# Optimization experiments

Hardware: AMD Instinct MI355X
Metric: run time of the kernel (lower is better)

## Reference

```python
import jax, jax.numpy as jnp
import numpy as np

B, S, D, H, FF = 2, 2048, 512, 8, 2048
DK = D // H
EPS = 1e-5


def layer_norm(x, g, b):
    mu = jnp.mean(x, axis=-1, keepdims=True)
    var = jnp.mean((x - mu) ** 2, axis=-1, keepdims=True)
    return (x - mu) / jnp.sqrt(var + EPS) * g + b


def split_heads(x):  # [B,S,D] -> [B,H,S,DK]
    b, s, _ = x.shape
    return x.reshape(b, s, H, DK).transpose(0, 2, 1, 3)


def merge_heads(x):  # [B,H,S,DK] -> [B,S,D]
    b, h, s, dk = x.shape
    return x.transpose(0, 2, 1, 3).reshape(b, s, h * dk)


def mha(q_in, kv, in_w, in_b, out_w, out_b):
    # torch nn.MultiheadAttention, batch_first, eval mode (no dropout)
    Wq, Wk, Wv = in_w[:D], in_w[D:2 * D], in_w[2 * D:]
    bq, bk, bv = in_b[:D], in_b[D:2 * D], in_b[2 * D:]
    q = split_heads(q_in @ Wq.T + bq)
    k = split_heads(kv @ Wk.T + bk)
    v = split_heads(kv @ Wv.T + bv)
    scores = jnp.einsum('bhqd,bhkd->bhqk', q, k) / jnp.sqrt(jnp.float32(DK))
    attn = jax.nn.softmax(scores, axis=-1)
    out = merge_heads(jnp.einsum('bhqk,bhkd->bhqd', attn, v))
    return out @ out_w.T + out_b


def setup_inputs() -> dict:
    key = jax.random.key(0)
    ks = jax.random.split(key, 32)
    p = lambda k, shape: (jax.random.normal(k, shape, jnp.float32) * 0.02)
    inp = {
        'x_q': jax.random.normal(ks[0], (B, S, D), jnp.float32),
        'x1': jax.random.normal(ks[1], (B, S, D), jnp.float32),
        'x2': jax.random.normal(ks[2], (B, S, D), jnp.float32),
        # causal self-attention projections (no output proj in original)
        'sa_wq': p(ks[3], (D, D)), 'sa_bq': jnp.zeros((D,), jnp.float32),
        'sa_wk': p(ks[4], (D, D)), 'sa_bk': jnp.zeros((D,), jnp.float32),
        'sa_wv': p(ks[5], (D, D)), 'sa_bv': jnp.zeros((D,), jnp.float32),
        'ln1_g': jnp.ones((D,), jnp.float32), 'ln1_b': jnp.zeros((D,), jnp.float32),
        # shared cross-attention (cross_attn used twice in forward)
        'mha_in_w': p(ks[6], (3 * D, D)), 'mha_in_b': jnp.zeros((3 * D,), jnp.float32),
        'mha_out_w': p(ks[7], (D, D)), 'mha_out_b': jnp.zeros((D,), jnp.float32),
        # shared add_norm2 (used twice)
        'ln2_g': jnp.ones((D,), jnp.float32), 'ln2_b': jnp.zeros((D,), jnp.float32),
        # FFN
        'ffn_w1': p(ks[8], (FF, D)), 'ffn_b1': jnp.zeros((FF,), jnp.float32),
        'ffn_w2': p(ks[9], (D, FF)), 'ffn_b2': jnp.zeros((D,), jnp.float32),
        # add_norm3 (final)
        'ln3_g': jnp.ones((D,), jnp.float32), 'ln3_b': jnp.zeros((D,), jnp.float32),
    }
    return inp


def reference(x_q, x1, x2, sa_wq, sa_bq, sa_wk, sa_bk, sa_wv, sa_bv,
              ln1_g, ln1_b, mha_in_w, mha_in_b, mha_out_w, mha_out_b,
              ln2_g, ln2_b, ffn_w1, ffn_b1, ffn_w2, ffn_b2, ln3_g, ln3_b):
    # --- causal self-attention (hand-rolled, masked_fill with -1e9) ---
    q = split_heads(x_q @ sa_wq.T + sa_bq)
    k = split_heads(x_q @ sa_wk.T + sa_bk)
    v = split_heads(x_q @ sa_wv.T + sa_bv)
    scores = jnp.einsum('bhqd,bhkd->bhqk', q, k) / jnp.sqrt(jnp.float32(DK))
    causal = jnp.tril(jnp.ones((S, S), dtype=bool))
    scores = jnp.where(causal[None, None], scores, jnp.float32(-1e9))
    attn = jax.nn.softmax(scores, axis=-1)
    y_sa = merge_heads(jnp.einsum('bhqk,bhkd->bhqd', attn, v))
    y = layer_norm(x_q + y_sa, ln1_g, ln1_b)
    # --- cross-attention 1 (shared weights) + shared add_norm2 ---
    yattn = mha(y, x1, mha_in_w, mha_in_b, mha_out_w, mha_out_b)
    yattn = layer_norm(y + yattn, ln2_g, ln2_b)
    # --- cross-attention 2 (SAME module/weights as cross-attn 1) ---
    yattn2 = mha(yattn, x2, mha_in_w, mha_in_b, mha_out_w, mha_out_b)
    yattn2 = layer_norm(yattn + yattn2, ln2_g, ln2_b)
    # --- FFN + add_norm3 ---
    h = jax.nn.relu(yattn2 @ ffn_w1.T + ffn_b1)
    ff = h @ ffn_w2.T + ffn_b2
    return layer_norm(yattn2 + ff, ln3_g, ln3_b)
```

## Files before the change

### kernel.cpp

```cpp
#include <hip/hip_runtime.h>
#include <hip/hip_bf16.h>

#define S_LEN 2048
#define DMODEL 512
#define NHEAD 8
#define DKH 64
#define FFDIM 2048
#define BATCH 2
#define NROWS (BATCH * S_LEN)

using bf16 = __hip_bfloat16;
typedef __bf16 bf16x8 __attribute__((ext_vector_type(8)));
typedef float floatx4 __attribute__((ext_vector_type(4)));
typedef float floatx16 __attribute__((ext_vector_type(16)));

__device__ inline unsigned short f2bf_bits(float f) {
    union { float f; unsigned u; } c; c.f = f;
    return (unsigned short)((c.u + 0x7FFFu + ((c.u >> 16) & 1u)) >> 16);
}
__device__ inline unsigned pack2bf(float a, float b) {
    return (unsigned)f2bf_bits(a) | ((unsigned)f2bf_bits(b) << 16);
}
__device__ inline unsigned pk2(float a, float b) {
    float2 f; f.x = a; f.y = b;
    __hip_bfloat162 h = __float22bfloat162_rn(f);
    return *(unsigned*)&h;
}

__device__ __forceinline__ void gload_lds16(const bf16* g, bf16* l) {
    __builtin_amdgcn_global_load_lds(
        (const __attribute__((address_space(1))) void*)(const void*)g,
        (__attribute__((address_space(3))) void*)(void*)l, 16, 0, 0);
}

struct CvtSeg { const float* s; bf16* d; int n4; };
struct CvtDesc { CvtSeg seg[12]; };

__launch_bounds__(256)
__global__ void cvt_f32_bf16(CvtDesc desc) {
    const CvtSeg sg = desc.seg[blockIdx.y];
    const int stride = gridDim.x * 256;
    for (int i = blockIdx.x * 256 + threadIdx.x; i < sg.n4; i += stride) {
        const float4 v = ((const float4*)sg.s)[i];
        uint2 o;
        o.x = pack2bf(v.x, v.y);
        o.y = pack2bf(v.z, v.w);
        ((uint2*)sg.d)[i] = o;
    }
}

struct Epi {
    bf16*  outB[3];
    float* outF[3];
    const float* bias[3];
    float scale[3];
    const bf16* A2;
    int a2slab;
    int shift;
    int relu;
};

template <int BM, int BN>
__launch_bounds__(256)
__global__ void gemm2(const bf16* __restrict__ A, const bf16* __restrict__ W,
                      Epi epi, int K)
{
    constexpr int WR = BM / 32;
    constexpr int WC = BN / 32;
    constexpr int SA = BM / 16;
    constexpr int SB = BN / 16;
    constexpr int NG = 2 * (SA + SB);

    __shared__ alignas(16) bf16 As[2][BM][32];
    __shared__ alignas(16) bf16 Bs[2][BN][32];

    const int t = threadIdx.x;
    const int w = t >> 6;
    const int lane = t & 63;
    const int r16 = lane & 15;
    const int quad = lane >> 4;
    const int wm = w >> 1, wn = w & 1;
    const int m0 = blockIdx.x * BM;
    const int n0 = blockIdx.y * BN;

    const bf16* Ause = (epi.A2 && ((n0 >> epi.shift) >= epi.a2slab)) ? epi.A2 : A;

    floatx4 acc[WR][WC];
#pragma unroll
    for (int i = 0; i < WR; i++)
#pragma unroll
        for (int j = 0; j < WC; j++)
#pragma unroll
            for (int e = 0; e < 4; e++) acc[i][j][e] = 0.0f;

    const int grow = lane >> 2;
    const int gcol = (lane & 3) * 8;

    for (int k0 = 0; k0 < K; k0 += 64) {
        __syncthreads();
#pragma unroll
        for (int s = 0; s < NG; s += 4) {
            int sg = s + w;
            int p = 0;
            if (sg >= SA + SB) { p = 1; sg -= SA + SB; }
            const bf16* src;
            bf16* dst;
            if (sg < SA) {
                src = Ause + (size_t)(m0 + sg * 16 + grow) * K + k0 + 32 * p + gcol;
                dst = &As[p][sg * 16][0] + lane * 8;
            } else {
                const int sb = sg - SA;
                src = W + (size_t)(n0 + sb * 16 + grow) * K + k0 + 32 * p + gcol;
                dst = &Bs[p][sb * 16][0] + lane * 8;
            }
            gload_lds16(src, dst);
        }
        __syncthreads();

        bf16x8 af[2][WR], bfr[2][WC];
#pragma unroll
        for (int p = 0; p < 2; p++) {
#pragma unroll
            for (int i = 0; i < WR; i++)
                af[p][i] = *(const bf16x8*)&As[p][wm * (BM / 2) + 16 * i + r16][quad * 8];
#pragma unroll
            for (int j = 0; j < WC; j++)
                bfr[p][j] = *(const bf16x8*)&Bs[p][wn * (BN / 2) + 16 * j + r16][quad * 8];
        }
#pragma unroll
        for (int p = 0; p < 2; p++)
#pragma unroll
            for (int i = 0; i < WR; i++)
#pragma unroll
                for (int j = 0; j < WC; j++)
                    acc[i][j] = __builtin_amdgcn_mfma_f32_16x16x32_bf16(af[p][i], bfr[p][j], acc[i][j], 0, 0, 0);
    }

    const int mask = (1 << epi.shift) - 1;
#pragma unroll
    for (int j = 0; j < WC; j++) {
        const int colb = n0 + wn * (BN / 2) + 16 * j;
        const int sel = __builtin_amdgcn_readfirstlane(colb >> epi.shift);
        const int lcol = (colb & mask) + r16;
        const int ldw = mask + 1;
        const float bv = epi.bias[sel] ? epi.bias[sel][lcol] : 0.0f;
        const float sc = epi.scale[sel];
        bf16* ob = epi.outB[sel];
        float* of = epi.outF[sel];
#pragma unroll
        for (int i = 0; i < WR; i++) {
            const int rowb = m0 + wm * (BM / 2) + 16 * i + 4 * quad;
#pragma unroll
            for (int e = 0; e < 4; e++) {
                float v = (acc[i][j][e] + bv) * sc;
                if (epi.relu) v = fmaxf(v, 0.0f);
                const size_t idx = (size_t)(rowb + e) * ldw + lcol;
                if (of) of[idx] = v;
                if (ob) ob[idx] = __float2bfloat16(v);
            }
        }
    }
}

#define PST 72

__launch_bounds__(256)
__global__ void attn_mfma(const bf16* __restrict__ Qh, const bf16* __restrict__ Kh,
                          const bf16* __restrict__ Vh,
                          float* __restrict__ outF, bf16* __restrict__ outB,
                          int causal)
{
    __shared__ alignas(16) char smem[36864];
    typedef bf16 (*VtT)[64][PST];
    typedef bf16 (*PsT)[32][PST];
    VtT Vt = (VtT)smem;
    PsT Ps = (PsT)(smem + 18432);
    typedef float (*MshT)[64][34];
    MshT Msh = (MshT)smem;

    const int t = threadIdx.x;
    const int w = t >> 6;
    const int lane = t & 63;
    const int c32 = lane & 31;
    const int hi = lane >> 5;
    const int pair = t >> 7;
    const int qg = w & 1;
    const int pl = t & 127;
    const int bh = blockIdx.y;
    const int b = bh >> 3, h = bh & 7;
    const int q0 = blockIdx.x * 64;
    const size_t rowbase = (size_t)b * S_LEN;
    const int hoff = h * DKH;

    bf16x8 qf[4];
    {
        const bf16* qp = Qh + (rowbase + q0 + 32 * qg + c32) * DMODEL + hoff + 8 * hi;
#pragma unroll
        for (int tt = 0; tt < 4; tt++) qf[tt] = *(const bf16x8*)(qp + 16 * tt);
    }

    floatx16 o0, o1;
#pragma unroll
    for (int e = 0; e < 16; e++) { o0[e] = 0.0f; o1[e] = 0.0f; }
    float m = -3e38f, l = 0.0f;

    const int rq = pl & 15;
    const int c8 = ((pl >> 4) & 7) * 8;

    const int nchunk = causal ? (q0 / 64 + 1) : (S_LEN / 64);
    const int nIter = (nchunk + 1) >> 1;

    bf16x8 kf0[4], kf1[4];
    if (pair < nchunk) {
        const bf16* kp = Kh + (rowbase + pair * 64 + c32) * DMODEL + hoff + 8 * hi;
#pragma unroll
        for (int tt = 0; tt < 4; tt++) {
            kf0[tt] = *(const bf16x8*)(kp + 16 * tt);
            kf1[tt] = *(const bf16x8*)(kp + (size_t)32 * DMODEL + 16 * tt);
        }
    }

    for (int it = 0; it < nIter; it++) {
        const int ch = 2 * it + pair;
        const bool active = ch < nchunk;
        const int kb = ch * 64;
        __syncthreads();
        if (active) {
            union { uint4 u; unsigned short s[8]; } r0, r1, r2, r3;
            const bf16* vb = Vh + (rowbase + kb + 4 * rq) * DMODEL + hoff + c8;
            r0.u = *(const uint4*)(vb);
            r1.u = *(const uint4*)(vb + DMODEL);
            r2.u = *(const uint4*)(vb + 2 * DMODEL);
            r3.u = *(const uint4*)(vb + 3 * DMODEL);
#pragma unroll
            for (int j = 0; j < 8; j++) {
                ushort4 pk = { r0.s[j], r1.s[j], r2.s[j], r3.s[j] };
                *(ushort4*)&Vt[pair][c8 + j][4 * rq] = pk;
            }
        }

        if (active) {
            floatx16 s0, s1;
#pragma unroll
            for (int e = 0; e < 16; e++) { s0[e] = 0.0f; s1[e] = 0.0f; }
#pragma unroll
            for (int tt = 0; tt < 4; tt++) {
                s0 = __builtin_amdgcn_mfma_f32_32x32x16_bf16(kf0[tt], qf[tt], s0, 0, 0, 0);
                s1 = __builtin_amdgcn_mfma_f32_32x32x16_bf16(kf1[tt], qf[tt], s1, 0, 0, 0);
            }

            const int chn = ch + 2;
            if (chn < nchunk) {
                const bf16* kp = Kh + (rowbase + chn * 64 + c32) * DMODEL + hoff + 8 * hi;
#pragma unroll
                for (int tt = 0; tt < 4; tt++) {
                    kf0[tt] = *(const bf16x8*)(kp + 16 * tt);
                    kf1[tt] = *(const bf16x8*)(kp + (size_t)32 * DMODEL + 16 * tt);
                }
            }

            if (causal && kb == q0) {
                const int qq = 32 * qg + c32;
#pragma unroll
                for (int r = 0; r < 16; r++) {
                    const int kl = (r & 3) + 8 * (r >> 2) + 4 * hi;
                    if (kl > qq) s0[r] = -3e38f;
                    if (kl + 32 > qq) s1[r] = -3e38f;
                }
            }

            float mc = -3e38f;
#pragma unroll
            for (int r = 0; r < 16; r++) mc = fmaxf(mc, fmaxf(s0[r], s1[r]));
            mc = fmaxf(mc, __shfl_xor(mc, 32, 64));
            const float mold = m;
            const float mn = fmaxf(m, mc);
            const float alpha = __expf(mold - mn);
            m = mn;

            float lc = 0.0f;
#pragma unroll
            for (int g = 0; g < 4; g++) {
                float p0 = __expf(s0[4 * g + 0] - mn), p1 = __expf(s0[4 * g + 1] - mn);
                float p2 = __expf(s0[4 * g + 2] - mn), p3 = __expf(s0[4 * g + 3] - mn);
                lc += (p0 + p1) + (p2 + p3);
                uint2 pw; pw.x = pk2(p0, p1); pw.y = pk2(p2, p3);
                *(uint2*)&Ps[w][c32][8 * g + 4 * hi] = pw;
                p0 = __expf(s1[4 * g + 0] - mn); p1 = __expf(s1[4 * g + 1] - mn);
                p2 = __expf(s1[4 * g + 2] - mn); p3 = __expf(s1[4 * g + 3] - mn);
                lc += (p0 + p1) + (p2 + p3);
                uint2 pw1; pw1.x = pk2(p0, p1); pw1.y = pk2(p2, p3);
                *(uint2*)&Ps[w][c32][32 + 8 * g + 4 * hi] = pw1;
            }
            lc += __shfl_xor(lc, 32, 64);
            l = l * alpha + lc;

            if (!__all(mn == mold)) {
#pragma unroll
                for (int r = 0; r < 16; r++) {
                    const float a = __shfl(alpha, (r & 3) + 8 * (r >> 2) + 4 * hi, 64);
                    o0[r] *= a; o1[r] *= a;
                }
            }
        }

        __syncthreads();

        if (active) {
#pragma unroll
            for (int tt = 0; tt < 4; tt++) {
                const bf16x8 pf = *(const bf16x8*)&Ps[w][c32][16 * tt + 8 * hi];
                const bf16x8 v0 = *(const bf16x8*)&Vt[pair][c32][16 * tt + 8 * hi];
                const bf16x8 v1 = *(const bf16x8*)&Vt[pair][32 + c32][16 * tt + 8 * hi];
                o0 = __builtin_amdgcn_mfma_f32_32x32x16_bf16(pf, v0, o0, 0, 0, 0);
                o1 = __builtin_amdgcn_mfma_f32_32x32x16_bf16(pf, v1, o1, 0, 0, 0);
            }
        }
    }

    __syncthreads();
    if (pair == 1) {
        float* dst = &Msh[qg][lane][0];
        dst[0] = m; dst[1] = l;
#pragma unroll
        for (int r = 0; r < 16; r++) { dst[2 + r] = o0[r]; dst[18 + r] = o1[r]; }
    }
    __syncthreads();
    if (pair == 0) {
        const float* src = &Msh[qg][lane][0];
        const float m_b = src[0], l_b = src[1];
        const float mt = fmaxf(m, m_b);
        const float sA = __expf(m - mt);
        const float sB = __expf(m_b - mt);
        const float lt = l * sA + l_b * sB;
#pragma unroll
        for (int r = 0; r < 16; r++) {
            const int ql = (r & 3) + 8 * (r >> 2) + 4 * hi;
            const float sAr = __shfl(sA, ql, 64);
            const float sBr = __shfl(sB, ql, 64);
            const float li = 1.0f / __shfl(lt, ql, 64);
            const float v0 = (o0[r] * sAr + src[2 + r] * sBr) * li;
            const float v1 = (o1[r] * sAr + src[18 + r] * sBr) * li;
            const size_t idx = (rowbase + q0 + 32 * qg + ql) * DMODEL + hoff + c32;
            if (outF) { outF[idx] = v0; outF[idx + 32] = v1; }
            if (outB) { outB[idx] = __float2bfloat16(v0); outB[idx + 32] = __float2bfloat16(v1); }
        }
    }
}

__launch_bounds__(256)
__global__ void ln_kernel(const float* __restrict__ xmain,
                          const float* __restrict__ resF, const bf16* __restrict__ resB,
                          const float* __restrict__ g, const float* __restrict__ bb,
                          float* __restrict__ outF, bf16* __restrict__ outB)
{
    const int row = blockIdx.x;
    const int t = threadIdx.x;
    const size_t base = (size_t)row * DMODEL;

    float x0 = xmain[base + t];
    float x1 = xmain[base + t + 256];
    if (resF) { x0 += resF[base + t]; x1 += resF[base + t + 256]; }
    if (resB) { x0 += __bfloat162float(resB[base + t]); x1 += __bfloat162float(resB[base + t + 256]); }

    __shared__ float sred[4];
    float s = x0 + x1;
#pragma unroll
    for (int off = 32; off > 0; off >>= 1) s += __shfl_down(s, off);
    if ((t & 63) == 0) sred[t >> 6] = s;
    __syncthreads();
    const float mu = (sred[0] + sred[1] + sred[2] + sred[3]) * (1.0f / DMODEL);

    const float d0 = x0 - mu, d1 = x1 - mu;
    float sv = d0 * d0 + d1 * d1;
#pragma unroll
    for (int off = 32; off > 0; off >>= 1) sv += __shfl_down(sv, off);
    __syncthreads();
    if ((t & 63) == 0) sred[t >> 6] = sv;
    __syncthreads();
    const float var = (sred[0] + sred[1] + sred[2] + sred[3]) * (1.0f / DMODEL);
    const float rstd = rsqrtf(var + 1e-5f);

    const float y0 = d0 * rstd * g[t] + bb[t];
    const float y1 = d1 * rstd * g[t + 256] + bb[t + 256];
    if (outF) { outF[base + t] = y0; outF[base + t + 256] = y1; }
    if (outB) { outB[base + t] = __float2bfloat16(y0); outB[base + t + 256] = __float2bfloat16(y1); }
}

extern "C" void kernel_launch(void* const* d_in, const int* in_sizes, int n_in,
                              void* d_out, int out_size, void* d_ws, size_t ws_size,
                              hipStream_t stream)
{
    const float* x_q       = (const float*)d_in[0];
    const float* x1        = (const float*)d_in[1];
    const float* x2        = (const float*)d_in[2];
    const float* sa_wq     = (const float*)d_in[3];
    const float* sa_bq     = (const float*)d_in[4];
    const float* sa_wk     = (const float*)d_in[5];
    const float* sa_bk     = (const float*)d_in[6];
    const float* sa_wv     = (const float*)d_in[7];
    const float* sa_bv     = (const float*)d_in[8];
    const float* ln1_g     = (const float*)d_in[9];
    const float* ln1_b     = (const float*)d_in[10];
    const float* mha_in_w  = (const float*)d_in[11];
    const float* mha_in_b  = (const float*)d_in[12];
    const float* mha_out_w = (const float*)d_in[13];
    const float* mha_out_b = (const float*)d_in[14];
    const float* ln2_g     = (const float*)d_in[15];
    const float* ln2_b     = (const float*)d_in[16];
    const float* ffn_w1    = (const float*)d_in[17];
    const float* ffn_b1    = (const float*)d_in[18];
    const float* ffn_w2    = (const float*)d_in[19];
    const float* ffn_b2    = (const float*)d_in[20];
    const float* ln3_g     = (const float*)d_in[21];
    const float* ln3_b     = (const float*)d_in[22];

    char* ws = (char*)d_ws;
    const size_t MB = 1024 * 1024;
    const size_t KB = 1024;
    bf16*  q16  = (bf16*)(ws + 0 * MB);
    bf16*  k16  = (bf16*)(ws + 4 * MB);
    bf16*  v16  = (bf16*)(ws + 8 * MB);
    bf16*  a16  = (bf16*)(ws + 12 * MB);
    float* tmp  = (float*)(ws + 16 * MB);
    bf16*  y16  = (bf16*)(ws + 24 * MB);
    bf16*  ya16 = (bf16*)(ws + 28 * MB);
    bf16*  ya2  = (bf16*)(ws + 32 * MB);
    bf16*  xq16 = (bf16*)(ws + 36 * MB);
    bf16*  x116 = (bf16*)(ws + 40 * MB);
    bf16*  x216 = (bf16*)(ws + 44 * MB);
    bf16*  w_sa_qkv = (bf16*)(ws + 48 * MB);
    bf16*  w_in   = (bf16*)(ws + 49 * MB + 512 * KB);
    bf16*  w_out  = (bf16*)(ws + 51 * MB);
    bf16*  w_f1   = (bf16*)(ws + 51 * MB + 512 * KB);
    bf16*  w_f2   = (bf16*)(ws + 53 * MB + 512 * KB);
    bf16*  h16    = (bf16*)(ws + 0 * MB);

    const int DD = DMODEL * DMODEL;
    CvtDesc cd;
    cd.seg[0]  = { x_q,       xq16,        (NROWS * DMODEL) / 4 };
    cd.seg[1]  = { x1,        x116,        (NROWS * DMODEL) / 4 };
    cd.seg[2]  = { x2,        x216,        (NROWS * DMODEL) / 4 };
    cd.seg[3]  = { sa_wq,     w_sa_qkv,           DD / 4 };
    cd.seg[4]  = { sa_wk,     w_sa_qkv + DD,      DD / 4 };
    cd.seg[5]  = { sa_wv,     w_sa_qkv + 2 * DD,  DD / 4 };
    cd.seg[6]  = { mha_in_w,  w_in,   3 * DD / 4 };
    cd.seg[7]  = { mha_out_w, w_out,  DD / 4 };
    cd.seg[8]  = { ffn_w1,    w_f1,   (FFDIM * DMODEL) / 4 };
    cd.seg[9]  = { ffn_w2,    w_f2,   (FFDIM * DMODEL) / 4 };
    cd.seg[10] = { x_q,       xq16,   0 };
    cd.seg[11] = { x_q,       xq16,   0 };
    cvt_f32_bf16<<<dim3(64, 10), 256, 0, stream>>>(cd);

    const dim3 blk(256);
    const dim3 agrid(S_LEN / 64, BATCH * NHEAD);

    Epi eQKV = {};
    eQKV.outB[0] = q16; eQKV.outB[1] = k16; eQKV.outB[2] = v16;
    eQKV.bias[0] = sa_bq; eQKV.bias[1] = sa_bk; eQKV.bias[2] = sa_bv;
    eQKV.scale[0] = 0.125f; eQKV.scale[1] = 1.0f; eQKV.scale[2] = 1.0f;
    eQKV.shift = 9;

    Epi eX1 = {};
    eX1.outB[0] = q16; eX1.outB[1] = k16; eX1.outB[2] = v16;
    eX1.bias[0] = mha_in_b; eX1.bias[1] = mha_in_b + DMODEL; eX1.bias[2] = mha_in_b + 2 * DMODEL;
    eX1.scale[0] = 0.125f; eX1.scale[1] = 1.0f; eX1.scale[2] = 1.0f;
    eX1.A2 = x116; eX1.a2slab = 1; eX1.shift = 9;

    Epi eX2 = eX1;
    eX2.A2 = x216;

    Epi eOut = {};
    eOut.outF[0] = tmp; eOut.bias[0] = mha_out_b; eOut.scale[0] = 1.0f; eOut.shift = 9;

    Epi eF1 = {};
    eF1.outB[0] = h16; eF1.bias[0] = ffn_b1; eF1.scale[0] = 1.0f;
    eF1.shift = 11; eF1.relu = 1;

    Epi eF2 = {};
    eF2.outF[0] = tmp; eF2.bias[0] = ffn_b2; eF2.scale[0] = 1.0f; eF2.shift = 9;

    gemm2<64, 64><<<dim3(64, 24), blk, 0, stream>>>(xq16, w_sa_qkv, eQKV, DMODEL);
    attn_mfma<<<agrid, blk, 0, stream>>>(q16, k16, v16, tmp, nullptr, 1);
    ln_kernel<<<NROWS, blk, 0, stream>>>(tmp, x_q, nullptr, ln1_g, ln1_b, nullptr, y16);

    gemm2<64, 64><<<dim3(64, 24), blk, 0, stream>>>(y16, w_in, eX1, DMODEL);
    attn_mfma<<<agrid, blk, 0, stream>>>(q16, k16, v16, nullptr, a16, 0);
    gemm2<64, 64><<<dim3(64, 8), blk, 0, stream>>>(a16, w_out, eOut, DMODEL);
    ln_kernel<<<NROWS, blk, 0, stream>>>(tmp, nullptr, y16, ln2_g, ln2_b, nullptr, ya16);

    gemm2<64, 64><<<dim3(64, 24), blk, 0, stream>>>(ya16, w_in, eX2, DMODEL);
    attn_mfma<<<agrid, blk, 0, stream>>>(q16, k16, v16, nullptr, a16, 0);
    gemm2<64, 64><<<dim3(64, 8), blk, 0, stream>>>(a16, w_out, eOut, DMODEL);
    ln_kernel<<<NROWS, blk, 0, stream>>>(tmp, nullptr, ya16, ln2_g, ln2_b, nullptr, ya2);

    gemm2<128, 128><<<dim3(32, 16), blk, 0, stream>>>(ya2, w_f1, eF1, DMODEL);
    gemm2<64, 64><<<dim3(64, 8), blk, 0, stream>>>(h16, w_f2, eF2, FFDIM);
    ln_kernel<<<NROWS, blk, 0, stream>>>(tmp, nullptr, ya2, ln3_g, ln3_b, (float*)d_out, nullptr);
}
```

Measured before the change: 447.5 us.

## Split attention key chunks across four wave pairs and keep softmax probabilities in registers

The attention kernel now runs 512 threads, so four wave pairs each process every fourth 64-key chunk, and their partial softmax states are merged in two rounds through shared memory. The P tile no longer goes through LDS: probabilities are packed to bf16 and rearranged across lanes with v_permlane32_swap to form the MFMA operand directly. The softmax switches to exp2 with log2(e) folded into the Q scale, and rescaling is skipped unless the running max grows by more than 8. MFMA sections are wrapped in s_setprio. This adds more merge work and more register pressure, and relies on the lane permutation matching the MFMA operand layout.

```diff
diff --git a/kernel.cpp b/kernel.cpp
--- a/kernel.cpp
+++ b/kernel.cpp
@@ -25,6 +25,9 @@
     float2 f; f.x = a; f.y = b;
     __hip_bfloat162 h = __float22bfloat162_rn(f);
     return *(unsigned*)&h;
+}
+__device__ inline void pl32swap(unsigned &a, unsigned &b) {
+    asm volatile("v_permlane32_swap_b32 %0, %1" : "+v"(a), "+v"(b));
 }
 
 __device__ __forceinline__ void gload_lds16(const bf16* g, bf16* l) {
@@ -164,7 +167,7 @@
 
 #define PST 72
 
-__launch_bounds__(256)
+__launch_bounds__(512, 4)
 __global__ void attn_mfma(const bf16* __restrict__ Qh, const bf16* __restrict__ Kh,
                           const bf16* __restrict__ Vh,
                           float* __restrict__ outF, bf16* __restrict__ outB,
@@ -172,10 +175,8 @@
 {
     __shared__ alignas(16) char smem[36864];
     typedef bf16 (*VtT)[64][PST];
-    typedef bf16 (*PsT)[32][PST];
     VtT Vt = (VtT)smem;
-    PsT Ps = (PsT)(smem + 18432);
-    typedef float (*MshT)[64][34];
+    typedef float (*MshT)[2][64][34];
     MshT Msh = (MshT)smem;
 
     const int t = threadIdx.x;
@@ -208,7 +209,7 @@
     const int c8 = ((pl >> 4) & 7) * 8;
 
     const int nchunk = causal ? (q0 / 64 + 1) : (S_LEN / 64);
-    const int nIter = (nchunk + 1) >> 1;
+    const int nIter = (nchunk + 3) >> 2;
 
     bf16x8 kf0[4], kf1[4];
     if (pair < nchunk) {
@@ -221,7 +222,7 @@
     }
 
     for (int it = 0; it < nIter; it++) {
-        const int ch = 2 * it + pair;
+        const int ch = 4 * it + pair;
         const bool active = ch < nchunk;
         const int kb = ch * 64;
         __syncthreads();
@@ -239,17 +240,20 @@
             }
         }
 
+        unsigned pw[16];
         if (active) {
             floatx16 s0, s1;
 #pragma unroll
             for (int e = 0; e < 16; e++) { s0[e] = 0.0f; s1[e] = 0.0f; }
+            __builtin_amdgcn_s_setprio(1);
 #pragma unroll
             for (int tt = 0; tt < 4; tt++) {
                 s0 = __builtin_amdgcn_mfma_f32_32x32x16_bf16(kf0[tt], qf[tt], s0, 0, 0, 0);
                 s1 = __builtin_amdgcn_mfma_f32_32x32x16_bf16(kf1[tt], qf[tt], s1, 0, 0, 0);
             }
-
-            const int chn = ch + 2;
+            __builtin_amdgcn_s_setprio(0);
+
+            const int chn = ch + 4;
             if (chn < nchunk) {
                 const bf16* kp = Kh + (rowbase + chn * 64 + c32) * DMODEL + hoff + 8 * hi;
 #pragma unroll
@@ -273,65 +277,102 @@
 #pragma unroll
             for (int r = 0; r < 16; r++) mc = fmaxf(mc, fmaxf(s0[r], s1[r]));
             mc = fmaxf(mc, __shfl_xor(mc, 32, 64));
-            const float mold = m;
-            const float mn = fmaxf(m, mc);
-            const float alpha = __expf(mold - mn);
-            m = mn;
-
-            float lc = 0.0f;
-#pragma unroll
-            for (int g = 0; g < 4; g++) {
-                float p0 = __expf(s0[4 * g + 0] - mn), p1 = __expf(s0[4 * g + 1] - mn);
-                float p2 = __expf(s0[4 * g + 2] - mn), p3 = __expf(s0[4 * g + 3] - mn);
-                lc += (p0 + p1) + (p2 + p3);
-                uint2 pw; pw.x = pk2(p0, p1); pw.y = pk2(p2, p3);
-                *(uint2*)&Ps[w][c32][8 * g + 4 * hi] = pw;
-                p0 = __expf(s1[4 * g + 0] - mn); p1 = __expf(s1[4 * g + 1] - mn);
-                p2 = __expf(s1[4 * g + 2] - mn); p3 = __expf(s1[4 * g + 3] - mn);
-                lc += (p0 + p1) + (p2 + p3);
-                uint2 pw1; pw1.x = pk2(p0, p1); pw1.y = pk2(p2, p3);
-                *(uint2*)&Ps[w][c32][32 + 8 * g + 4 * hi] = pw1;
-            }
-            lc += __shfl_xor(lc, 32, 64);
-            l = l * alpha + lc;
-
-            if (!__all(mn == mold)) {
+
+            float alpha = 1.0f;
+            if (!__all(mc <= m + 8.0f)) {
+                const float mold = m;
+                m = fmaxf(m, mc);
+                alpha = __builtin_amdgcn_exp2f(mold - m);
 #pragma unroll
                 for (int r = 0; r < 16; r++) {
                     const float a = __shfl(alpha, (r & 3) + 8 * (r >> 2) + 4 * hi, 64);
                     o0[r] *= a; o1[r] *= a;
                 }
             }
+
+            float lc = 0.0f;
+#pragma unroll
+            for (int half = 0; half < 2; half++) {
+                floatx16& sv = half ? s1 : s0;
+#pragma unroll
+                for (int g = 0; g < 2; g++) {
+                    float p[8];
+#pragma unroll
+                    for (int r = 0; r < 8; r++) {
+                        p[r] = __builtin_amdgcn_exp2f(sv[8 * g + r] - m);
+                        lc += p[r];
+                    }
+                    unsigned A0 = pk2(p[0], p[1]);
+                    unsigned A1 = pk2(p[2], p[3]);
+                    unsigned B0 = pk2(p[4], p[5]);
+                    unsigned B1 = pk2(p[6], p[7]);
+                    pl32swap(A0, B0);
+                    pl32swap(A1, B1);
+                    const int tt = 2 * half + g;
+                    pw[4 * tt + 0] = A0; pw[4 * tt + 1] = A1;
+                    pw[4 * tt + 2] = B0; pw[4 * tt + 3] = B1;
+                }
+            }
+            lc += __shfl_xor(lc, 32, 64);
+            l = l * alpha + lc;
         }
 
         __syncthreads();
 
         if (active) {
+            __builtin_amdgcn_s_setprio(1);
 #pragma unroll
             for (int tt = 0; tt < 4; tt++) {
-                const bf16x8 pf = *(const bf16x8*)&Ps[w][c32][16 * tt + 8 * hi];
+                union { unsigned u[4]; bf16x8 v; } pu;
+                pu.u[0] = pw[4 * tt + 0]; pu.u[1] = pw[4 * tt + 1];
+                pu.u[2] = pw[4 * tt + 2]; pu.u[3] = pw[4 * tt + 3];
                 const bf16x8 v0 = *(const bf16x8*)&Vt[pair][c32][16 * tt + 8 * hi];
                 const bf16x8 v1 = *(const bf16x8*)&Vt[pair][32 + c32][16 * tt + 8 * hi];
-                o0 = __builtin_amdgcn_mfma_f32_32x32x16_bf16(pf, v0, o0, 0, 0, 0);
-                o1 = __builtin_amdgcn_mfma_f32_32x32x16_bf16(pf, v1, o1, 0, 0, 0);
-            }
+                o0 = __builtin_amdgcn_mfma_f32_32x32x16_bf16(pu.v, v0, o0, 0, 0, 0);
+                o1 = __builtin_amdgcn_mfma_f32_32x32x16_bf16(pu.v, v1, o1, 0, 0, 0);
+            }
+            __builtin_amdgcn_s_setprio(0);
         }
     }
 
     __syncthreads();
-    if (pair == 1) {
-        float* dst = &Msh[qg][lane][0];
+    if (pair & 1) {
+        float* dst = &Msh[pair >> 1][qg][lane][0];
         dst[0] = m; dst[1] = l;
 #pragma unroll
         for (int r = 0; r < 16; r++) { dst[2 + r] = o0[r]; dst[18 + r] = o1[r]; }
+    }
+    __syncthreads();
+    if ((pair & 1) == 0) {
+        const float* src = &Msh[pair >> 1][qg][lane][0];
+        const float m_b = src[0], l_b = src[1];
+        const float mt = fmaxf(m, m_b);
+        const float sA = __builtin_amdgcn_exp2f(m - mt);
+        const float sB = __builtin_amdgcn_exp2f(m_b - mt);
+        l = l * sA + l_b * sB;
+        m = mt;
+#pragma unroll
+        for (int r = 0; r < 16; r++) {
+            const int ql = (r & 3) + 8 * (r >> 2) + 4 * hi;
+            const float sAr = __shfl(sA, ql, 64);
+            const float sBr = __shfl(sB, ql, 64);
+            o0[r] = o0[r] * sAr + src[2 + r] * sBr;
+            o1[r] = o1[r] * sAr + src[18 + r] * sBr;
+        }
+        if (pair == 2) {
+            float* dst = &Msh[1][qg][lane][0];
+            dst[0] = m; dst[1] = l;
+#pragma unroll
+            for (int r = 0; r < 16; r++) { dst[2 + r] = o0[r]; dst[18 + r] = o1[r]; }
+        }
     }
     __syncthreads();
     if (pair == 0) {
-        const float* src = &Msh[qg][lane][0];
+        const float* src = &Msh[1][qg][lane][0];
         const float m_b = src[0], l_b = src[1];
         const float mt = fmaxf(m, m_b);
-        const float sA = __expf(m - mt);
-        const float sB = __expf(m_b - mt);
+        const float sA = __builtin_amdgcn_exp2f(m - mt);
+        const float sB = __builtin_amdgcn_exp2f(m_b - mt);
         const float lt = l * sA + l_b * sB;
 #pragma unroll
         for (int r = 0; r < 16; r++) {
@@ -453,18 +494,21 @@
     cvt_f32_bf16<<<dim3(64, 10), 256, 0, stream>>>(cd);
 
     const dim3 blk(256);
+    const dim3 ablk(512);
     const dim3 agrid(S_LEN / 64, BATCH * NHEAD);
+
+    const float QSC = 0.125f * 1.44269504088896f;
 
     Epi eQKV = {};
     eQKV.outB[0] = q16; eQKV.outB[1] = k16; eQKV.outB[2] = v16;
     eQKV.bias[0] = sa_bq; eQKV.bias[1] = sa_bk; eQKV.bias[2] = sa_bv;
-    eQKV.scale[0] = 0.125f; eQKV.scale[1] = 1.0f; eQKV.scale[2] = 1.0f;
+    eQKV.scale[0] = QSC; eQKV.scale[1] = 1.0f; eQKV.scale[2] = 1.0f;
     eQKV.shift = 9;
 
     Epi eX1 = {};
     eX1.outB[0] = q16; eX1.outB[1] = k16; eX1.outB[2] = v16;
     eX1.bias[0] = mha_in_b; eX1.bias[1] = mha_in_b + DMODEL; eX1.bias[2] = mha_in_b + 2 * DMODEL;
-    eX1.scale[0] = 0.125f; eX1.scale[1] = 1.0f; eX1.scale[2] = 1.0f;
+    eX1.scale[0] = QSC; eX1.scale[1] = 1.0f; eX1.scale[2] = 1.0f;
     eX1.A2 = x116; eX1.a2slab = 1; eX1.shift = 9;
 
     Epi eX2 = eX1;
@@ -481,16 +525,16 @@
     eF2.outF[0] = tmp; eF2.bias[0] = ffn_b2; eF2.scale[0] = 1.0f; eF2.shift = 9;
 
     gemm2<64, 64><<<dim3(64, 24), blk, 0, stream>>>(xq16, w_sa_qkv, eQKV, DMODEL);
-    attn_mfma<<<agrid, blk, 0, stream>>>(q16, k16, v16, tmp, nullptr, 1);
+    attn_mfma<<<agrid, ablk, 0, stream>>>(q16, k16, v16, tmp, nullptr, 1);
     ln_kernel<<<NROWS, blk, 0, stream>>>(tmp, x_q, nullptr, ln1_g, ln1_b, nullptr, y16);
 
     gemm2<64, 64><<<dim3(64, 24), blk, 0, stream>>>(y16, w_in, eX1, DMODEL);
-    attn_mfma<<<agrid, blk, 0, stream>>>(q16, k16, v16, nullptr, a16, 0);
+    attn_mfma<<<agrid, ablk, 0, stream>>>(q16, k16, v16, nullptr, a16, 0);
     gemm2<64, 64><<<dim3(64, 8), blk, 0, stream>>>(a16, w_out, eOut, DMODEL);
     ln_kernel<<<NROWS, blk, 0, stream>>>(tmp, nullptr, y16, ln2_g, ln2_b, nullptr, ya16);
 
     gemm2<64, 64><<<dim3(64, 24), blk, 0, stream>>>(ya16, w_in, eX2, DMODEL);
-    attn_mfma<<<agrid, blk, 0, stream>>>(q16, k16, v16, nullptr, a16, 0);
+    attn_mfma<<<agrid, ablk, 0, stream>>>(q16, k16, v16, nullptr, a16, 0);
     gemm2<64, 64><<<dim3(64, 8), blk, 0, stream>>>(a16, w_out, eOut, DMODEL);
     ln_kernel<<<NROWS, blk, 0, stream>>>(tmp, nullptr, ya16, ln2_g, ln2_b, nullptr, ya2);
 
```

After: 685.8 us. 53.3% more time.

## Restructure attention into 512-thread blocks with shared K/V tiles and exp2 softmax

Applied to the files above, without the earlier changes.

The attention kernel now handles 128 queries per block with 8 waves, split into four query groups and two key halves per 64-key chunk. K is staged once in shared memory for all waves instead of each wave loading it from global memory into registers. The softmax uses exp2 with log2e folded into the Q scale, skips the rescale when the new max stays within a threshold of the old one, and raises wave priority around MFMA sections. The cost is two barriers per chunk and lost register prefetch of K, with grid size halved to 256 blocks, which may reduce occupancy.

```diff
diff --git a/kernel.cpp b/kernel.cpp
--- a/kernel.cpp
+++ b/kernel.cpp
@@ -162,18 +162,20 @@
     }
 }
 
-#define PST 72
-
-__launch_bounds__(256)
+#define KST 72
+#define PST2 44
+
+__launch_bounds__(512, 2)
 __global__ void attn_mfma(const bf16* __restrict__ Qh, const bf16* __restrict__ Kh,
                           const bf16* __restrict__ Vh,
                           float* __restrict__ outF, bf16* __restrict__ outB,
                           int causal)
 {
-    __shared__ alignas(16) char smem[36864];
-    typedef bf16 (*VtT)[64][PST];
-    typedef bf16 (*PsT)[32][PST];
-    VtT Vt = (VtT)smem;
+    __shared__ alignas(16) char smem[40960];
+    typedef bf16 (*KsT)[KST];
+    KsT Ks = (KsT)smem;
+    KsT Vt = (KsT)(smem + 9216);
+    typedef bf16 (*PsT)[32][PST2];
     PsT Ps = (PsT)(smem + 18432);
     typedef float (*MshT)[64][34];
     MshT Msh = (MshT)smem;
@@ -183,18 +185,17 @@
     const int lane = t & 63;
     const int c32 = lane & 31;
     const int hi = lane >> 5;
-    const int pair = t >> 7;
-    const int qg = w & 1;
-    const int pl = t & 127;
+    const int qg = w >> 1;
+    const int kh = w & 1;
     const int bh = blockIdx.y;
     const int b = bh >> 3, h = bh & 7;
-    const int q0 = blockIdx.x * 64;
+    const int q0 = blockIdx.x * 128;
     const size_t rowbase = (size_t)b * S_LEN;
     const int hoff = h * DKH;
 
     bf16x8 qf[4];
     {
-        const bf16* qp = Qh + (rowbase + q0 + 32 * qg + c32) * DMODEL + hoff + 8 * hi;
+        const bf16* qp = Qh + (rowbase + q0 + qg * 32 + c32) * DMODEL + hoff + 8 * hi;
 #pragma unroll
         for (int tt = 0; tt < 4; tt++) qf[tt] = *(const bf16x8*)(qp + 16 * tt);
     }
@@ -204,28 +205,25 @@
     for (int e = 0; e < 16; e++) { o0[e] = 0.0f; o1[e] = 0.0f; }
     float m = -3e38f, l = 0.0f;
 
+    const int krow = t >> 3;
+    const int kcol = (t & 7) * 8;
+    const int pl = t - 256;
     const int rq = pl & 15;
     const int c8 = ((pl >> 4) & 7) * 8;
 
-    const int nchunk = causal ? (q0 / 64 + 1) : (S_LEN / 64);
-    const int nIter = (nchunk + 1) >> 1;
-
-    bf16x8 kf0[4], kf1[4];
-    if (pair < nchunk) {
-        const bf16* kp = Kh + (rowbase + pair * 64 + c32) * DMODEL + hoff + 8 * hi;
-#pragma unroll
-        for (int tt = 0; tt < 4; tt++) {
-            kf0[tt] = *(const bf16x8*)(kp + 16 * tt);
-            kf1[tt] = *(const bf16x8*)(kp + (size_t)32 * DMODEL + 16 * tt);
-        }
-    }
-
-    for (int it = 0; it < nIter; it++) {
-        const int ch = 2 * it + pair;
-        const bool active = ch < nchunk;
+    const int nchunk = causal ? (q0 / 64 + 2) : (S_LEN / 64);
+
+    for (int ch = 0; ch < nchunk; ch++) {
         const int kb = ch * 64;
         __syncthreads();
-        if (active) {
+
+        if (t < 256) {
+            const bf16* kp = Kh + (rowbase + kb + krow) * DMODEL + hoff + kcol;
+            uint4 ka = *(const uint4*)(kp);
+            uint4 kc = *(const uint4*)(kp + (size_t)32 * DMODEL);
+            *(uint4*)&Ks[krow][kcol] = ka;
+            *(uint4*)&Ks[krow + 32][kcol] = kc;
+        } else if (t < 384) {
             union { uint4 u; unsigned short s[8]; } r0, r1, r2, r3;
             const bf16* vb = Vh + (rowbase + kb + 4 * rq) * DMODEL + hoff + c8;
             r0.u = *(const uint4*)(vb);
@@ -235,103 +233,92 @@
 #pragma unroll
             for (int j = 0; j < 8; j++) {
                 ushort4 pk = { r0.s[j], r1.s[j], r2.s[j], r3.s[j] };
-                *(ushort4*)&Vt[pair][c8 + j][4 * rq] = pk;
+                *(ushort4*)&Vt[c8 + j][4 * rq] = pk;
             }
         }
 
-        if (active) {
-            floatx16 s0, s1;
-#pragma unroll
-            for (int e = 0; e < 16; e++) { s0[e] = 0.0f; s1[e] = 0.0f; }
-#pragma unroll
-            for (int tt = 0; tt < 4; tt++) {
-                s0 = __builtin_amdgcn_mfma_f32_32x32x16_bf16(kf0[tt], qf[tt], s0, 0, 0, 0);
-                s1 = __builtin_amdgcn_mfma_f32_32x32x16_bf16(kf1[tt], qf[tt], s1, 0, 0, 0);
+        __syncthreads();
+
+        bf16x8 kf[4];
+#pragma unroll
+        for (int tt = 0; tt < 4; tt++)
+            kf[tt] = *(const bf16x8*)&Ks[kh * 32 + c32][16 * tt + 8 * hi];
+
+        floatx16 s;
+#pragma unroll
+        for (int e = 0; e < 16; e++) s[e] = 0.0f;
+        __builtin_amdgcn_s_setprio(1);
+#pragma unroll
+        for (int tt = 0; tt < 4; tt++)
+            s = __builtin_amdgcn_mfma_f32_32x32x16_bf16(kf[tt], qf[tt], s, 0, 0, 0);
+        __builtin_amdgcn_s_setprio(0);
+
+        if (causal && ch >= nchunk - 2) {
+            const int qq = q0 + qg * 32 + c32;
+#pragma unroll
+            for (int r = 0; r < 16; r++) {
+                const int kl = kb + kh * 32 + (r & 3) + 8 * (r >> 2) + 4 * hi;
+                if (kl > qq) s[r] = -3e38f;
             }
-
-            const int chn = ch + 2;
-            if (chn < nchunk) {
-                const bf16* kp = Kh + (rowbase + chn * 64 + c32) * DMODEL + hoff + 8 * hi;
-#pragma unroll
-                for (int tt = 0; tt < 4; tt++) {
-                    kf0[tt] = *(const bf16x8*)(kp + 16 * tt);
-                    kf1[tt] = *(const bf16x8*)(kp + (size_t)32 * DMODEL + 16 * tt);
-                }
+        }
+
+        float mc = -3e38f;
+#pragma unroll
+        for (int r = 0; r < 16; r++) mc = fmaxf(mc, s[r]);
+        mc = fmaxf(mc, __shfl_xor(mc, 32, 64));
+
+        float alpha = 1.0f;
+        if (!__all(mc <= m + 8.0f)) {
+            const float mold = m;
+            m = fmaxf(m, mc);
+            alpha = __builtin_amdgcn_exp2f(mold - m);
+#pragma unroll
+            for (int r = 0; r < 16; r++) {
+                const float a = __shfl(alpha, (r & 3) + 8 * (r >> 2) + 4 * hi, 64);
+                o0[r] *= a; o1[r] *= a;
             }
-
-            if (causal && kb == q0) {
-                const int qq = 32 * qg + c32;
-#pragma unroll
-                for (int r = 0; r < 16; r++) {
-                    const int kl = (r & 3) + 8 * (r >> 2) + 4 * hi;
-                    if (kl > qq) s0[r] = -3e38f;
-                    if (kl + 32 > qq) s1[r] = -3e38f;
-                }
-            }
-
-            float mc = -3e38f;
-#pragma unroll
-            for (int r = 0; r < 16; r++) mc = fmaxf(mc, fmaxf(s0[r], s1[r]));
-            mc = fmaxf(mc, __shfl_xor(mc, 32, 64));
-            const float mold = m;
-            const float mn = fmaxf(m, mc);
-            const float alpha = __expf(mold - mn);
-            m = mn;
-
-            float lc = 0.0f;
-#pragma unroll
-            for (int g = 0; g < 4; g++) {
-                float p0 = __expf(s0[4 * g + 0] - mn), p1 = __expf(s0[4 * g + 1] - mn);
-                float p2 = __expf(s0[4 * g + 2] - mn), p3 = __expf(s0[4 * g + 3] - mn);
-                lc += (p0 + p1) + (p2 + p3);
-                uint2 pw; pw.x = pk2(p0, p1); pw.y = pk2(p2, p3);
-                *(uint2*)&Ps[w][c32][8 * g + 4 * hi] = pw;
-                p0 = __expf(s1[4 * g + 0] - mn); p1 = __expf(s1[4 * g + 1] - mn);
-                p2 = __expf(s1[4 * g + 2] - mn); p3 = __expf(s1[4 * g + 3] - mn);
-                lc += (p0 + p1) + (p2 + p3);
-                uint2 pw1; pw1.x = pk2(p0, p1); pw1.y = pk2(p2, p3);
-                *(uint2*)&Ps[w][c32][32 + 8 * g + 4 * hi] = pw1;
-            }
-            lc += __shfl_xor(lc, 32, 64);
-            l = l * alpha + lc;
-
-            if (!__all(mn == mold)) {
-#pragma unroll
-                for (int r = 0; r < 16; r++) {
-                    const float a = __shfl(alpha, (r & 3) + 8 * (r >> 2) + 4 * hi, 64);
-                    o0[r] *= a; o1[r] *= a;
-                }
-            }
-        }
-
-        __syncthreads();
-
-        if (active) {
-#pragma unroll
-            for (int tt = 0; tt < 4; tt++) {
-                const bf16x8 pf = *(const bf16x8*)&Ps[w][c32][16 * tt + 8 * hi];
-                const bf16x8 v0 = *(const bf16x8*)&Vt[pair][c32][16 * tt + 8 * hi];
-                const bf16x8 v1 = *(const bf16x8*)&Vt[pair][32 + c32][16 * tt + 8 * hi];
-                o0 = __builtin_amdgcn_mfma_f32_32x32x16_bf16(pf, v0, o0, 0, 0, 0);
-                o1 = __builtin_amdgcn_mfma_f32_32x32x16_bf16(pf, v1, o1, 0, 0, 0);
-            }
-        }
+        }
+
+        float lc = 0.0f;
+#pragma unroll
+        for (int g = 0; g < 4; g++) {
+            float p0 = __builtin_amdgcn_exp2f(s[4 * g + 0] - m);
+            float p1 = __builtin_amdgcn_exp2f(s[4 * g + 1] - m);
+            float p2 = __builtin_amdgcn_exp2f(s[4 * g + 2] - m);
+            float p3 = __builtin_amdgcn_exp2f(s[4 * g + 3] - m);
+            lc += (p0 + p1) + (p2 + p3);
+            uint2 pw; pw.x = pk2(p0, p1); pw.y = pk2(p2, p3);
+            *(uint2*)&Ps[w][c32][8 * g + 4 * hi] = pw;
+        }
+        lc += __shfl_xor(lc, 32, 64);
+        l = l * alpha + lc;
+
+        __builtin_amdgcn_s_setprio(1);
+#pragma unroll
+        for (int tt = 0; tt < 2; tt++) {
+            const bf16x8 pf = *(const bf16x8*)&Ps[w][c32][16 * tt + 8 * hi];
+            const bf16x8 v0 = *(const bf16x8*)&Vt[c32][kh * 32 + 16 * tt + 8 * hi];
+            const bf16x8 v1 = *(const bf16x8*)&Vt[32 + c32][kh * 32 + 16 * tt + 8 * hi];
+            o0 = __builtin_amdgcn_mfma_f32_32x32x16_bf16(pf, v0, o0, 0, 0, 0);
+            o1 = __builtin_amdgcn_mfma_f32_32x32x16_bf16(pf, v1, o1, 0, 0, 0);
+        }
+        __builtin_amdgcn_s_setprio(0);
     }
 
     __syncthreads();
-    if (pair == 1) {
+    if (kh == 1) {
         float* dst = &Msh[qg][lane][0];
         dst[0] = m; dst[1] = l;
 #pragma unroll
         for (int r = 0; r < 16; r++) { dst[2 + r] = o0[r]; dst[18 + r] = o1[r]; }
     }
     __syncthreads();
-    if (pair == 0) {
+    if (kh == 0) {
         const float* src = &Msh[qg][lane][0];
         const float m_b = src[0], l_b = src[1];
         const float mt = fmaxf(m, m_b);
-        const float sA = __expf(m - mt);
-        const float sB = __expf(m_b - mt);
+        const float sA = __builtin_amdgcn_exp2f(m - mt);
+        const float sB = __builtin_amdgcn_exp2f(m_b - mt);
         const float lt = l * sA + l_b * sB;
 #pragma unroll
         for (int r = 0; r < 16; r++) {
@@ -341,7 +328,7 @@
             const float li = 1.0f / __shfl(lt, ql, 64);
             const float v0 = (o0[r] * sAr + src[2 + r] * sBr) * li;
             const float v1 = (o1[r] * sAr + src[18 + r] * sBr) * li;
-            const size_t idx = (rowbase + q0 + 32 * qg + ql) * DMODEL + hoff + c32;
+            const size_t idx = (rowbase + q0 + qg * 32 + ql) * DMODEL + hoff + c32;
             if (outF) { outF[idx] = v0; outF[idx + 32] = v1; }
             if (outB) { outB[idx] = __float2bfloat16(v0); outB[idx + 32] = __float2bfloat16(v1); }
         }
@@ -453,18 +440,21 @@
     cvt_f32_bf16<<<dim3(64, 10), 256, 0, stream>>>(cd);
 
     const dim3 blk(256);
-    const dim3 agrid(S_LEN / 64, BATCH * NHEAD);
+    const dim3 ablk(512);
+    const dim3 agrid(S_LEN / 128, BATCH * NHEAD);
+
+    const float QSC = 0.125f * 1.44269504088896f;
 
     Epi eQKV = {};
     eQKV.outB[0] = q16; eQKV.outB[1] = k16; eQKV.outB[2] = v16;
     eQKV.bias[0] = sa_bq; eQKV.bias[1] = sa_bk; eQKV.bias[2] = sa_bv;
-    eQKV.scale[0] = 0.125f; eQKV.scale[1] = 1.0f; eQKV.scale[2] = 1.0f;
+    eQKV.scale[0] = QSC; eQKV.scale[1] = 1.0f; eQKV.scale[2] = 1.0f;
     eQKV.shift = 9;
 
     Epi eX1 = {};
     eX1.outB[0] = q16; eX1.outB[1] = k16; eX1.outB[2] = v16;
     eX1.bias[0] = mha_in_b; eX1.bias[1] = mha_in_b + DMODEL; eX1.bias[2] = mha_in_b + 2 * DMODEL;
-    eX1.scale[0] = 0.125f; eX1.scale[1] = 1.0f; eX1.scale[2] = 1.0f;
+    eX1.scale[0] = QSC; eX1.scale[1] = 1.0f; eX1.scale[2] = 1.0f;
     eX1.A2 = x116; eX1.a2slab = 1; eX1.shift = 9;
 
     Epi eX2 = eX1;
@@ -481,16 +471,16 @@
     eF2.outF[0] = tmp; eF2.bias[0] = ffn_b2; eF2.scale[0] = 1.0f; eF2.shift = 9;
 
     gemm2<64, 64><<<dim3(64, 24), blk, 0, stream>>>(xq16, w_sa_qkv, eQKV, DMODEL);
-    attn_mfma<<<agrid, blk, 0, stream>>>(q16, k16, v16, tmp, nullptr, 1);
+    attn_mfma<<<agrid, ablk, 0, stream>>>(q16, k16, v16, tmp, nullptr, 1);
     ln_kernel<<<NROWS, blk, 0, stream>>>(tmp, x_q, nullptr, ln1_g, ln1_b, nullptr, y16);
 
     gemm2<64, 64><<<dim3(64, 24), blk, 0, stream>>>(y16, w_in, eX1, DMODEL);
-    attn_mfma<<<agrid, blk, 0, stream>>>(q16, k16, v16, nullptr, a16, 0);
+    attn_mfma<<<agrid, ablk, 0, stream>>>(q16, k16, v16, nullptr, a16, 0);
     gemm2<64, 64><<<dim3(64, 8), blk, 0, stream>>>(a16, w_out, eOut, DMODEL);
     ln_kernel<<<NROWS, blk, 0, stream>>>(tmp, nullptr, y16, ln2_g, ln2_b, nullptr, ya16);
 
     gemm2<64, 64><<<dim3(64, 24), blk, 0, stream>>>(ya16, w_in, eX2, DMODEL);
-    attn_mfma<<<agrid, blk, 0, stream>>>(q16, k16, v16, nullptr, a16, 0);
+    attn_mfma<<<agrid, ablk, 0, stream>>>(q16, k16, v16, nullptr, a16, 0);
     gemm2<64, 64><<<dim3(64, 8), blk, 0, stream>>>(a16, w_out, eOut, DMODEL);
     ln_kernel<<<NROWS, blk, 0, stream>>>(tmp, nullptr, ya16, ln2_g, ln2_b, nullptr, ya2);
 
```

After: 443.1 us. No clear change (-1.0%).
